# Kernel optimization log

Measured on AMD Instinct MI355X. Metric: run time of the kernel, lower is better.

Reference implementation:

```python
import jax, jax.numpy as jnp
import numpy as np

N, E, D, L = 50000, 600000, 128, 3
EPS = 1e-5


def _layer_norm(x, g, b):
    m = jnp.mean(x, axis=-1, keepdims=True)
    v = jnp.mean((x - m) ** 2, axis=-1, keepdims=True)
    return (x - m) * jax.lax.rsqrt(v + EPS) * g + b


def setup_inputs() -> dict:
    key = jax.random.key(0)
    ks = jax.random.split(key, 20)
    s = 1.0 / np.sqrt(D)
    inp = {
        "node": jax.random.normal(ks[0], (N, D), jnp.float32),
        "edge_attr": jax.random.uniform(ks[1], (E,), jnp.float32),
        # stacked per-layer parameters [L, ...]
        "W_rel": jax.random.uniform(ks[2], (L, D, D), jnp.float32, -s, s),
        "b_rel": jax.random.uniform(ks[3], (L, D), jnp.float32, -s, s),
        "W_root": jax.random.uniform(ks[4], (L, D, D), jnp.float32, -s, s),
        "ln1_g": jnp.ones((L, D), jnp.float32),
        "ln1_b": jnp.zeros((L, D), jnp.float32),
        "ln2_g": jnp.ones((L, D), jnp.float32),
        "ln2_b": jnp.zeros((L, D), jnp.float32),
        "W1": jax.random.uniform(ks[5], (L, D, D), jnp.float32, -s, s),
        "b1": jax.random.uniform(ks[6], (L, D), jnp.float32, -s, s),
        "W2": jax.random.uniform(ks[7], (L, D, D), jnp.float32, -s, s),
        "b2": jax.random.uniform(ks[8], (L, D), jnp.float32, -s, s),
        "jk_W": jax.random.uniform(ks[9], (L * D, D), jnp.float32, -1.0 / np.sqrt(L * D), 1.0 / np.sqrt(L * D)),
        "jk_b": jax.random.uniform(ks[10], (D,), jnp.float32, -1.0 / np.sqrt(L * D), 1.0 / np.sqrt(L * D)),
        "edge_index": jax.random.randint(ks[11], (2, E), 0, N, jnp.int64),
        "batch_ptr": jnp.sort(jax.random.randint(ks[12], (51,), 0, N, jnp.int64)),
    }
    return inp


def reference(node, edge_attr, W_rel, b_rel, W_root, ln1_g, ln1_b, ln2_g, ln2_b,
              W1, b1, W2, b2, jk_W, jk_b, edge_index, batch_ptr):
    src, dst = edge_index[0], edge_index[1]
    deg = jax.ops.segment_sum(jnp.ones((E,), node.dtype), dst, num_segments=N)
    inv_deg = 1.0 / jnp.maximum(deg, 1.0)  # nodes with no in-edges -> 0 aggregate
    outs = []
    for l in range(L):
        msg = node[src] * edge_attr[:, None]                       # [E, D] gather
        agg = jax.ops.segment_sum(msg, dst, num_segments=N)        # scatter-sum
        mean = agg * inv_deg[:, None]                              # mean aggregation
        # GraphConv: lin_rel(aggr) + lin_root(x); skip_connection=False
        node = mean @ W_rel[l] + b_rel[l] + node @ W_root[l]
        node = jax.nn.relu(_layer_norm(node @ W1[l] + b1[l], ln1_g[l], ln1_b[l]))
        node = jax.nn.relu(_layer_norm(node @ W2[l] + b2[l], ln2_g[l], ln2_b[l]))
        outs.append(node)
    jk = jnp.concatenate(outs, axis=-1)                            # [N, L*D]
    return jk @ jk_W + jk_b
```

## Files before the change

kernel.cpp:

```cpp
#include <hip/hip_runtime.h>

#define NN 50000
#define EE 600000
#define DD 128
#define CAP 64
#define SLDS_STRIDE 66
#define BINS 196
#define NP (BINS * 256)
#define BINCAP 3584
#define BCSTRIDE 16
#define LDS_STRIDE 136
#define P1_EDGES 2048
#define P1_BLOCKS ((EE + P1_EDGES - 1) / P1_EDGES)
#define CONV_BLKS 6250
#define PREP_BLKS (97 + CONV_BLKS)

typedef __attribute__((ext_vector_type(8))) short bf16x8;
typedef __attribute__((ext_vector_type(4))) float f32x4;

__device__ __forceinline__ unsigned short f2bf(float f) {
    union { float f; unsigned u; } v; v.f = f;
    unsigned r = v.u + 0x7FFF + ((v.u >> 16) & 1);
    return (unsigned short)(r >> 16);
}
__device__ __forceinline__ float bflo(unsigned x) { return __uint_as_float(x << 16); }
__device__ __forceinline__ float bfhi(unsigned x) { return __uint_as_float(x & 0xffff0000u); }

__global__ __launch_bounds__(256) void prep_fill(
    const float* __restrict__ nodef, unsigned short* __restrict__ node_bf,
    const float* __restrict__ W_rel, const float* __restrict__ W_root,
    const float* __restrict__ W1, const float* __restrict__ W2,
    const float* __restrict__ jkW,
    const float* __restrict__ b_rel, const float* __restrict__ b1,
    float* __restrict__ bc, unsigned short* __restrict__ packed,
    const int* __restrict__ src, const int* __restrict__ dst, const float* __restrict__ ea,
    int* __restrict__ binCnt, unsigned long long* __restrict__ recs) {
    __shared__ int hist[BINS];
    __shared__ int lstart[BINS];
    __shared__ int gbase[BINS];
    __shared__ int scan[256];
    __shared__ unsigned long long srt[P1_EDGES];
    const int b = blockIdx.x;
    const int t = threadIdx.x;

    if (b < 96) {
        int tg = b * 256 + t;
        int chunk = tg >> 11, r = tg & 2047;
        int lane = r & 63, tile = r >> 6;
        int kt = tile >> 3, nt = tile & 7;
        int quad = lane >> 4, n = lane & 15;
        int k0 = kt * 32 + quad * 8;
        int col = nt * 16 + n;
        union { unsigned short u[8]; uint4 v; } tmp;
        if (chunk < 6) {
            int l = (chunk < 3) ? chunk : chunk - 3;
            const float* A = ((chunk < 3) ? W_rel : W_root) + (size_t)l * 16384;
            const float* B = W1 + (size_t)l * 16384;
            float acc[8] = {0.f, 0.f, 0.f, 0.f, 0.f, 0.f, 0.f, 0.f};
            for (int k = 0; k < 128; ++k) {
                float bv = B[k * 128 + col];
#pragma unroll
                for (int j = 0; j < 8; ++j) acc[j] = fmaf(A[(k0 + j) * 128 + k], bv, acc[j]);
            }
#pragma unroll
            for (int j = 0; j < 8; ++j) tmp.u[j] = f2bf(acc[j]);
        } else {
            const float* s = (chunk < 9) ? (W2 + (size_t)(chunk - 6) * 16384)
                                         : (jkW + (size_t)(chunk - 9) * 16384);
#pragma unroll
            for (int j = 0; j < 8; ++j) tmp.u[j] = f2bf(s[(size_t)(k0 + j) * DD + col]);
        }
        *(uint4*)&packed[(size_t)tg * 8] = tmp.v;
        return;
    } else if (b == 96) {
        for (int o = t; o < 384; o += 256) {
            int l = o >> 7, j = o & 127;
            float s = 0.f;
            for (int k = 0; k < 128; ++k)
                s = fmaf(b_rel[l * 128 + k], W1[(size_t)l * 16384 + k * 128 + j], s);
            bc[o] = s + b1[o];
        }
        return;
    } else if (b < PREP_BLKS) {
        int i = (b - 97) * 256 + t;
        float4 v = *(const float4*)&nodef[(size_t)i * 4];
        ushort4 o;
        o.x = f2bf(v.x); o.y = f2bf(v.y); o.z = f2bf(v.z); o.w = f2bf(v.w);
        *(ushort4*)&node_bf[(size_t)i * 4] = o;
        return;
    }

    const int pb = b - PREP_BLKS;
    for (int i = t; i < BINS; i += 256) hist[i] = 0;
    __syncthreads();

    unsigned long long rec[8];
    int bin[8], rnk[8];
    bool val[8];
#pragma unroll
    for (int g = 0; g < 2; ++g) {
        int e0 = pb * P1_EDGES + g * 1024 + t * 4;
        int4 dv, sv; float4 ev;
        if (e0 + 3 < EE) {
            dv = *(const int4*)&dst[e0];
            sv = *(const int4*)&src[e0];
            ev = *(const float4*)&ea[e0];
        } else {
            int* dp = (int*)&dv; int* sp = (int*)&sv; float* ep = (float*)&ev;
#pragma unroll
            for (int k = 0; k < 4; ++k) {
                int e = e0 + k;
                dp[k] = (e < EE) ? dst[e] : 0;
                sp[k] = (e < EE) ? src[e] : 0;
                ep[k] = (e < EE) ? ea[e] : 0.f;
            }
        }
#pragma unroll
        for (int k = 0; k < 4; ++k) {
            int i = g * 4 + k;
            int e = e0 + k;
            val[i] = (e < EE);
            int d = ((const int*)&dv)[k];
            unsigned w16 = (unsigned)__float2int_rn(((const float*)&ev)[k] * 65535.0f);
            if (w16 > 65535u) w16 = 65535u;
            rec[i] = ((unsigned long long)(unsigned)d << 32) |
                     (((unsigned)((const int*)&sv)[k]) << 16) | w16;
            bin[i] = d >> 8;
            rnk[i] = val[i] ? atomicAdd(&hist[bin[i]], 1) : 0;
        }
    }
    __syncthreads();
    scan[t] = (t < BINS) ? hist[t] : 0;
    __syncthreads();
#pragma unroll
    for (int off = 1; off < 256; off <<= 1) {
        int v = (t >= off) ? scan[t - off] : 0;
        __syncthreads();
        scan[t] += v;
        __syncthreads();
    }
    if (t < BINS) {
        lstart[t] = scan[t] - hist[t];
        gbase[t] = hist[t] ? atomicAdd(&binCnt[t * BCSTRIDE], hist[t]) : 0;
    }
    __syncthreads();
#pragma unroll
    for (int i = 0; i < 8; ++i)
        if (val[i]) srt[lstart[bin[i]] + rnk[i]] = rec[i];
    __syncthreads();
    const int total = scan[255];
    for (int j = t; j < total; j += 256) {
        unsigned long long r = srt[j];
        int bb = (int)(r >> 40);
        int o = gbase[bb] + (j - lstart[bb]);
        if (o < BINCAP) recs[(size_t)bb * BINCAP + o] = r;
    }
}

__global__ __launch_bounds__(256) void fill_p2(
    const int* __restrict__ binCnt, const unsigned long long* __restrict__ recs,
    int* __restrict__ cnt, unsigned* __restrict__ slots) {
    __shared__ int cl[128];
    __shared__ unsigned sl[128 * CAP];
    const int b = blockIdx.x >> 1, half = blockIdx.x & 1, t = threadIdx.x;
    if (t < 128) cl[t] = 0;
    __syncthreads();
    int n = binCnt[b * BCSTRIDE];
    if (n > BINCAP) n = BINCAP;
    const unsigned long long* rp = recs + (size_t)b * BINCAP;
    for (int j = t; j < n; j += 256) {
        unsigned long long r = rp[j];
        int dl = (int)(r >> 32) & 255;
        if ((dl >> 7) == half) {
            int p = atomicAdd(&cl[dl & 127], 1);
            if (p < CAP) sl[(dl & 127) * CAP + p] = (unsigned)r;
        }
    }
    __syncthreads();
    const int node0 = (b << 8) + (half << 7);
    if (t < 128) cnt[node0 + t] = cl[t];
    const uint4* s4 = (const uint4*)sl;
    uint4* g4 = (uint4*)(slots + (size_t)node0 * CAP);
    for (int i = t; i < 2048; i += 256) g4[i] = s4[i];
}

template <bool JK>
__global__ __launch_bounds__(64, 4) void fused_layer(
    const unsigned short* __restrict__ feat,
    const unsigned* __restrict__ slots, const int* __restrict__ cnt,
    const unsigned short* __restrict__ PWrel, const unsigned short* __restrict__ PWroot,
    const unsigned short* __restrict__ PW2,
    const float* __restrict__ bc, const float* __restrict__ ln1g, const float* __restrict__ ln1b,
    const float* __restrict__ b2, const float* __restrict__ ln2g, const float* __restrict__ ln2b,
    unsigned short* __restrict__ out,
    const unsigned short* __restrict__ o0, const unsigned short* __restrict__ o1,
    const unsigned short* __restrict__ PJ0, const unsigned short* __restrict__ PJ1,
    const unsigned short* __restrict__ PJ2,
    const float* __restrict__ jkb, float* __restrict__ fout) {
    __shared__ __align__(16) unsigned short wt[16 * LDS_STRIDE];
    __shared__ __align__(16) unsigned slds[16 * SLDS_STRIDE];
    const int lane = threadIdx.x;
    const int mrow = blockIdx.x * 16;
    const int quad = lane >> 4, n15 = lane & 15;
    const int kq   = quad * 8;
    const int i8   = n15 * 8;
    const float wscale = 1.0f / 65535.0f;

    const int cl0 = cnt[mrow + n15];
    const int cAll = (cl0 > CAP) ? CAP : cl0;

    {
        const unsigned* sbase = slots + (size_t)mrow * CAP;
#pragma unroll
        for (int k = 0; k < 4; ++k) {
            int li = k * 64 + lane;
            uint4 v = *(const uint4*)&sbase[li * 4];
            int rw = li >> 4, cu = (li & 15) * 4;
            *(uint4*)&slds[rw * SLDS_STRIDE + cu] = v;
        }
    }

    const unsigned short* An = feat + (size_t)(mrow + n15) * DD;
    bf16x8 an4[4];
#pragma unroll
    for (int kt = 0; kt < 4; ++kt) an4[kt] = *(const bf16x8*)&An[kt * 32 + kq];

    __asm__ __volatile__("s_waitcnt lgkmcnt(0)" ::: "memory");

#pragma unroll
    for (int r = 0; r < 4; ++r) {
        const int row = r * 4 + quad;
        int c = __shfl(cAll, row);
        float acc[8] = {0.f, 0.f, 0.f, 0.f, 0.f, 0.f, 0.f, 0.f};
        for (int j0 = 0; j0 < c; j0 += 4) {
            uint4 sv = *(const uint4*)&slds[row * SLDS_STRIDE + j0];
            unsigned se[4] = {sv.x, sv.y, sv.z, sv.w};
#pragma unroll
            for (int tt = 0; tt < 4; ++tt) {
                bool ok = (j0 + tt) < c;
                unsigned e = se[tt];
                int   srcn = ok ? (int)(e >> 16) : 0;
                float w    = ok ? (float)(e & 0xffffu) * wscale : 0.0f;
                uint4 v = *(const uint4*)&feat[(size_t)srcn * DD + i8];
                acc[0] = fmaf(bflo(v.x), w, acc[0]);
                acc[1] = fmaf(bfhi(v.x), w, acc[1]);
                acc[2] = fmaf(bflo(v.y), w, acc[2]);
                acc[3] = fmaf(bfhi(v.y), w, acc[3]);
                acc[4] = fmaf(bflo(v.z), w, acc[4]);
                acc[5] = fmaf(bfhi(v.z), w, acc[5]);
                acc[6] = fmaf(bflo(v.w), w, acc[6]);
                acc[7] = fmaf(bfhi(v.w), w, acc[7]);
            }
        }
        float id = 1.0f / fmaxf((float)c, 1.0f);
        union { unsigned short u[8]; uint4 v; } o;
#pragma unroll
        for (int k = 0; k < 8; ++k) o.u[k] = f2bf(acc[k] * id);
        *(uint4*)&wt[row * LDS_STRIDE + i8] = o.v;
    }
    __asm__ __volatile__("s_waitcnt lgkmcnt(0)" ::: "memory");

    f32x4 acc[8];
#pragma unroll
    for (int nt = 0; nt < 8; ++nt) acc[nt] = (f32x4){0.f, 0.f, 0.f, 0.f};
    __builtin_amdgcn_s_setprio(1);
#pragma unroll
    for (int kt = 0; kt < 4; ++kt) {
        bf16x8 am = *(const bf16x8*)&wt[n15 * LDS_STRIDE + kt * 32 + kq];
#pragma unroll
        for (int nt = 0; nt < 8; ++nt) {
            bf16x8 brel = *(const bf16x8*)&PWrel[(size_t)((kt * 8 + nt) * 64 + lane) * 8];
            acc[nt] = __builtin_amdgcn_mfma_f32_16x16x32_bf16(am, brel, acc[nt], 0, 0, 0);
            bf16x8 brt = *(const bf16x8*)&PWroot[(size_t)((kt * 8 + nt) * 64 + lane) * 8];
            acc[nt] = __builtin_amdgcn_mfma_f32_16x16x32_bf16(an4[kt], brt, acc[nt], 0, 0, 0);
        }
    }
    __builtin_amdgcn_s_setprio(0);

    float x[8][4];
#pragma unroll
    for (int nt = 0; nt < 8; ++nt) {
        float bv = bc[nt * 16 + n15];
#pragma unroll
        for (int r = 0; r < 4; ++r) x[nt][r] = acc[nt][r] + bv;
    }
    {
        float s[4] = {0, 0, 0, 0}, q[4] = {0, 0, 0, 0};
#pragma unroll
        for (int nt = 0; nt < 8; ++nt)
#pragma unroll
            for (int r = 0; r < 4; ++r) { s[r] += x[nt][r]; q[r] += x[nt][r] * x[nt][r]; }
#pragma unroll
        for (int m = 1; m <= 8; m <<= 1)
#pragma unroll
            for (int r = 0; r < 4; ++r) { s[r] += __shfl_xor(s[r], m); q[r] += __shfl_xor(q[r], m); }
        const float inv = 1.0f / 128.0f;
#pragma unroll
        for (int r = 0; r < 4; ++r) {
            float mu = s[r] * inv;
            float rs = rsqrtf(fmaxf(q[r] * inv - mu * mu, 0.0f) + 1e-5f);
#pragma unroll
            for (int nt = 0; nt < 8; ++nt) {
                float g = ln1g[nt * 16 + n15], bb = ln1b[nt * 16 + n15];
                x[nt][r] = fmaxf((x[nt][r] - mu) * rs * g + bb, 0.0f);
            }
        }
    }

#pragma unroll
    for (int nt = 0; nt < 8; ++nt)
#pragma unroll
        for (int r = 0; r < 4; ++r)
            wt[(quad * 4 + r) * LDS_STRIDE + nt * 16 + n15] = f2bf(x[nt][r]);
    __asm__ __volatile__("s_waitcnt lgkmcnt(0)" ::: "memory");

    f32x4 acc2[8];
#pragma unroll
    for (int nt = 0; nt < 8; ++nt) acc2[nt] = (f32x4){0.f, 0.f, 0.f, 0.f};
    __builtin_amdgcn_s_setprio(1);
#pragma unroll
    for (int kt = 0; kt < 4; ++kt) {
        bf16x8 ah = *(const bf16x8*)&wt[n15 * LDS_STRIDE + kt * 32 + kq];
#pragma unroll
        for (int nt = 0; nt < 8; ++nt) {
            bf16x8 bw = *(const bf16x8*)&PW2[(size_t)((kt * 8 + nt) * 64 + lane) * 8];
            acc2[nt] = __builtin_amdgcn_mfma_f32_16x16x32_bf16(ah, bw, acc2[nt], 0, 0, 0);
        }
    }
    __builtin_amdgcn_s_setprio(0);
#pragma unroll
    for (int nt = 0; nt < 8; ++nt) {
        float bv = b2[nt * 16 + n15];
#pragma unroll
        for (int r = 0; r < 4; ++r) x[nt][r] = acc2[nt][r] + bv;
    }
    {
        float s[4] = {0, 0, 0, 0}, q[4] = {0, 0, 0, 0};
#pragma unroll
        for (int nt = 0; nt < 8; ++nt)
#pragma unroll
            for (int r = 0; r < 4; ++r) { s[r] += x[nt][r]; q[r] += x[nt][r] * x[nt][r]; }
#pragma unroll
        for (int m = 1; m <= 8; m <<= 1)
#pragma unroll
            for (int r = 0; r < 4; ++r) { s[r] += __shfl_xor(s[r], m); q[r] += __shfl_xor(q[r], m); }
        const float inv = 1.0f / 128.0f;
#pragma unroll
        for (int r = 0; r < 4; ++r) {
            float mu = s[r] * inv;
            float rs = rsqrtf(fmaxf(q[r] * inv - mu * mu, 0.0f) + 1e-5f);
#pragma unroll
            for (int nt = 0; nt < 8; ++nt) {
                float g = ln2g[nt * 16 + n15], bb = ln2b[nt * 16 + n15];
                x[nt][r] = fmaxf((x[nt][r] - mu) * rs * g + bb, 0.0f);
            }
        }
    }

    __asm__ __volatile__("s_waitcnt lgkmcnt(0)" ::: "memory");
#pragma unroll
    for (int nt = 0; nt < 8; ++nt)
#pragma unroll
        for (int r = 0; r < 4; ++r)
            wt[(quad * 4 + r) * LDS_STRIDE + nt * 16 + n15] = f2bf(x[nt][r]);
    __asm__ __volatile__("s_waitcnt lgkmcnt(0)" ::: "memory");

    if constexpr (!JK) {
#pragma unroll
        for (int i = 0; i < 4; ++i) {
            int s = i * 512 + lane * 8;
            int r = s >> 7, col = s & 127;
            uint4 v = *(const uint4*)&wt[r * LDS_STRIDE + col];
            *(uint4*)&out[(size_t)(mrow + r) * DD + col] = v;
        }
    } else {
        f32x4 accJ[8];
#pragma unroll
        for (int nt = 0; nt < 8; ++nt) accJ[nt] = (f32x4){0.f, 0.f, 0.f, 0.f};
        __builtin_amdgcn_s_setprio(1);
#pragma unroll
        for (int kt = 0; kt < 4; ++kt) {
            bf16x8 ah = *(const bf16x8*)&wt[n15 * LDS_STRIDE + kt * 32 + kq];
#pragma unroll
            for (int nt = 0; nt < 8; ++nt) {
                bf16x8 bw = *(const bf16x8*)&PJ2[(size_t)((kt * 8 + nt) * 64 + lane) * 8];
                accJ[nt] = __builtin_amdgcn_mfma_f32_16x16x32_bf16(ah, bw, accJ[nt], 0, 0, 0);
            }
        }
        const unsigned short* A0 = o0 + (size_t)(mrow + n15) * DD;
        const unsigned short* A1 = o1 + (size_t)(mrow + n15) * DD;
#pragma unroll
        for (int kt = 0; kt < 4; ++kt) {
            bf16x8 a0 = *(const bf16x8*)&A0[kt * 32 + kq];
            bf16x8 a1 = *(const bf16x8*)&A1[kt * 32 + kq];
#pragma unroll
            for (int nt = 0; nt < 8; ++nt) {
                bf16x8 b0 = *(const bf16x8*)&PJ0[(size_t)((kt * 8 + nt) * 64 + lane) * 8];
                accJ[nt] = __builtin_amdgcn_mfma_f32_16x16x32_bf16(a0, b0, accJ[nt], 0, 0, 0);
                bf16x8 b1 = *(const bf16x8*)&PJ1[(size_t)((kt * 8 + nt) * 64 + lane) * 8];
                accJ[nt] = __builtin_amdgcn_mfma_f32_16x16x32_bf16(a1, b1, accJ[nt], 0, 0, 0);
            }
        }
        __builtin_amdgcn_s_setprio(0);
#pragma unroll
        for (int nt = 0; nt < 8; ++nt) {
            float bv = jkb[nt * 16 + n15];
#pragma unroll
            for (int r = 0; r < 4; ++r)
                fout[(size_t)(mrow + quad * 4 + r) * DD + nt * 16 + n15] = accJ[nt][r] + bv;
        }
    }
}

extern "C" void kernel_launch(void* const* d_in, const int* in_sizes, int n_in,
                              void* d_out, int out_size, void* d_ws, size_t ws_size,
                              hipStream_t stream) {
    const float* node   = (const float*)d_in[0];
    const float* ea     = (const float*)d_in[1];
    const float* W_rel  = (const float*)d_in[2];
    const float* b_rel  = (const float*)d_in[3];
    const float* W_root = (const float*)d_in[4];
    const float* ln1_g  = (const float*)d_in[5];
    const float* ln1_b  = (const float*)d_in[6];
    const float* ln2_g  = (const float*)d_in[7];
    const float* ln2_b  = (const float*)d_in[8];
    const float* W1     = (const float*)d_in[9];
    const float* b1     = (const float*)d_in[10];
    const float* W2     = (const float*)d_in[11];
    const float* b2     = (const float*)d_in[12];
    const float* jk_W   = (const float*)d_in[13];
    const float* jk_b   = (const float*)d_in[14];
    const int*   ei     = (const int*)d_in[15];
    const int* srcI = ei;
    const int* dstI = ei + EE;

    char* ws = (char*)d_ws;
    size_t off = 0;
    auto alloc = [&](size_t bytes) {
        void* p = ws + off;
        off += (bytes + 255) & ~(size_t)255;
        return p;
    };
    int*                binCnt  = (int*)alloc((size_t)BINS * BCSTRIDE * 4);
    unsigned long long* recs    = (unsigned long long*)alloc((size_t)BINS * BINCAP * 8);
    int*                cnt     = (int*)alloc((size_t)NP * 4);
    unsigned*           slots   = (unsigned*)alloc((size_t)NP * CAP * 4);
    unsigned short*     node_bf = (unsigned short*)alloc((size_t)NN * DD * 2);
    unsigned short* outs_bf[2];
    for (int l = 0; l < 2; ++l) outs_bf[l] = (unsigned short*)alloc((size_t)NN * DD * 2);
    float*              bc      = (float*)alloc((size_t)3 * 128 * 4);
    unsigned short*     packed  = (unsigned short*)alloc((size_t)12 * 16384 * 2);

    hipMemsetAsync(binCnt, 0, (size_t)BINS * BCSTRIDE * 4, stream);
    prep_fill<<<PREP_BLKS + P1_BLOCKS, 256, 0, stream>>>(
        node, node_bf, W_rel, W_root, W1, W2, jk_W, b_rel, b1, bc, packed,
        srcI, dstI, ea, binCnt, recs);
    fill_p2<<<BINS * 2, 256, 0, stream>>>(binCnt, recs, cnt, slots);

    const int gblocks = NN / 16;
    unsigned short* cur = node_bf;
    for (int l = 0; l < 3; ++l) {
        if (l < 2) {
            fused_layer<false><<<gblocks, 64, 0, stream>>>(
                cur, slots, cnt,
                packed + (size_t)l * 16384, packed + (size_t)(3 + l) * 16384,
                packed + (size_t)(6 + l) * 16384,
                bc + (size_t)l * DD, ln1_g + (size_t)l * DD, ln1_b + (size_t)l * DD,
                b2 + (size_t)l * DD, ln2_g + (size_t)l * DD, ln2_b + (size_t)l * DD,
                outs_bf[l],
                nullptr, nullptr, nullptr, nullptr, nullptr, nullptr, nullptr);
            cur = outs_bf[l];
        } else {
            fused_layer<true><<<gblocks, 64, 0, stream>>>(
                cur, slots, cnt,
                packed + (size_t)l * 16384, packed + (size_t)(3 + l) * 16384,
                packed + (size_t)(6 + l) * 16384,
                bc + (size_t)l * DD, ln1_g + (size_t)l * DD, ln1_b + (size_t)l * DD,
                b2 + (size_t)l * DD, ln2_g + (size_t)l * DD, ln2_b + (size_t)l * DD,
                nullptr,
                outs_bf[0], outs_bf[1],
                packed + (size_t)9 * 16384, packed + (size_t)10 * 16384, packed + (size_t)11 * 16384,
                jk_b, (float*)d_out);
        }
    }
}
```

Before: 248.7 us.

## Fuse three layer launches into one persistent kernel with grid barriers

The three per-layer kernel launches are replaced by a single kernel that loops over the layers in-kernel. A software grid barrier separates the layers: 64 spread atomic counters, spin-polled with s_sleep and bracketed by thread fences. The aim is to remove the launch gaps and tail effects between layers, and to load each block's neighbor-slot table into LDS once instead of once per layer. In exchange it depends on all 3125 blocks being co-resident, and it risks deadlock or spin overhead if occupancy is lower than assumed.

New measurement: 967.0 us. 3.89x slower.

```diff
diff --git a/kernel.cpp b/kernel.cpp
--- a/kernel.cpp
+++ b/kernel.cpp
@@ -14,6 +14,7 @@
 #define P1_BLOCKS ((EE + P1_EDGES - 1) / P1_EDGES)
 #define CONV_BLKS 6250
 #define PREP_BLKS (97 + CONV_BLKS)
+#define GBLOCKS (NN / 16)
 
 typedef __attribute__((ext_vector_type(8))) short bf16x8;
 typedef __attribute__((ext_vector_type(4))) float f32x4;
@@ -25,6 +26,15 @@
 }
 __device__ __forceinline__ float bflo(unsigned x) { return __uint_as_float(x << 16); }
 __device__ __forceinline__ float bfhi(unsigned x) { return __uint_as_float(x & 0xffff0000u); }
+
+__device__ __forceinline__ void gbar(int* bar, int lane, int bid) {
+    __threadfence();
+    if (lane == 0) atomicAdd(&bar[bid & 63], 1);
+    const int expct = (lane < 53) ? 49 : 48;
+    while (__hip_atomic_load(&bar[lane], __ATOMIC_RELAXED, __HIP_MEMORY_SCOPE_AGENT) < expct)
+        __builtin_amdgcn_s_sleep(16);
+    __threadfence();
+}
 
 __global__ __launch_bounds__(256) void prep_fill(
     const float* __restrict__ nodef, unsigned short* __restrict__ node_bf,
@@ -184,23 +194,19 @@
     for (int i = t; i < 2048; i += 256) g4[i] = s4[i];
 }
 
-template <bool JK>
-__global__ __launch_bounds__(64, 4) void fused_layer(
-    const unsigned short* __restrict__ feat,
+__global__ __launch_bounds__(64, 4) void fused_all(
+    const unsigned short* __restrict__ node_bf,
     const unsigned* __restrict__ slots, const int* __restrict__ cnt,
-    const unsigned short* __restrict__ PWrel, const unsigned short* __restrict__ PWroot,
-    const unsigned short* __restrict__ PW2,
-    const float* __restrict__ bc, const float* __restrict__ ln1g, const float* __restrict__ ln1b,
-    const float* __restrict__ b2, const float* __restrict__ ln2g, const float* __restrict__ ln2b,
-    unsigned short* __restrict__ out,
-    const unsigned short* __restrict__ o0, const unsigned short* __restrict__ o1,
-    const unsigned short* __restrict__ PJ0, const unsigned short* __restrict__ PJ1,
-    const unsigned short* __restrict__ PJ2,
-    const float* __restrict__ jkb, float* __restrict__ fout) {
+    const unsigned short* __restrict__ packed,
+    const float* __restrict__ bcA, const float* __restrict__ ln1gA, const float* __restrict__ ln1bA,
+    const float* __restrict__ b2A, const float* __restrict__ ln2gA, const float* __restrict__ ln2bA,
+    unsigned short* __restrict__ out0, unsigned short* __restrict__ out1,
+    const float* __restrict__ jkb, float* __restrict__ fout, int* __restrict__ bars) {
     __shared__ __align__(16) unsigned short wt[16 * LDS_STRIDE];
     __shared__ __align__(16) unsigned slds[16 * SLDS_STRIDE];
     const int lane = threadIdx.x;
-    const int mrow = blockIdx.x * 16;
+    const int bid  = blockIdx.x;
+    const int mrow = bid * 16;
     const int quad = lane >> 4, n15 = lane & 15;
     const int kq   = quad * 8;
     const int i8   = n15 * 8;
@@ -220,194 +226,212 @@
         }
     }
 
-    const unsigned short* An = feat + (size_t)(mrow + n15) * DD;
-    bf16x8 an4[4];
-#pragma unroll
-    for (int kt = 0; kt < 4; ++kt) an4[kt] = *(const bf16x8*)&An[kt * 32 + kq];
-
-    __asm__ __volatile__("s_waitcnt lgkmcnt(0)" ::: "memory");
-
-#pragma unroll
-    for (int r = 0; r < 4; ++r) {
-        const int row = r * 4 + quad;
-        int c = __shfl(cAll, row);
-        float acc[8] = {0.f, 0.f, 0.f, 0.f, 0.f, 0.f, 0.f, 0.f};
-        for (int j0 = 0; j0 < c; j0 += 4) {
-            uint4 sv = *(const uint4*)&slds[row * SLDS_STRIDE + j0];
-            unsigned se[4] = {sv.x, sv.y, sv.z, sv.w};
-#pragma unroll
-            for (int tt = 0; tt < 4; ++tt) {
-                bool ok = (j0 + tt) < c;
-                unsigned e = se[tt];
-                int   srcn = ok ? (int)(e >> 16) : 0;
-                float w    = ok ? (float)(e & 0xffffu) * wscale : 0.0f;
-                uint4 v = *(const uint4*)&feat[(size_t)srcn * DD + i8];
-                acc[0] = fmaf(bflo(v.x), w, acc[0]);
-                acc[1] = fmaf(bfhi(v.x), w, acc[1]);
-                acc[2] = fmaf(bflo(v.y), w, acc[2]);
-                acc[3] = fmaf(bfhi(v.y), w, acc[3]);
-                acc[4] = fmaf(bflo(v.z), w, acc[4]);
-                acc[5] = fmaf(bfhi(v.z), w, acc[5]);
-                acc[6] = fmaf(bflo(v.w), w, acc[6]);
-                acc[7] = fmaf(bfhi(v.w), w, acc[7]);
-            }
-        }
-        float id = 1.0f / fmaxf((float)c, 1.0f);
-        union { unsigned short u[8]; uint4 v; } o;
-#pragma unroll
-        for (int k = 0; k < 8; ++k) o.u[k] = f2bf(acc[k] * id);
-        *(uint4*)&wt[row * LDS_STRIDE + i8] = o.v;
-    }
-    __asm__ __volatile__("s_waitcnt lgkmcnt(0)" ::: "memory");
-
-    f32x4 acc[8];
-#pragma unroll
-    for (int nt = 0; nt < 8; ++nt) acc[nt] = (f32x4){0.f, 0.f, 0.f, 0.f};
-    __builtin_amdgcn_s_setprio(1);
-#pragma unroll
-    for (int kt = 0; kt < 4; ++kt) {
-        bf16x8 am = *(const bf16x8*)&wt[n15 * LDS_STRIDE + kt * 32 + kq];
+    for (int l = 0; l < 3; ++l) {
+        const unsigned short* feat  = (l == 0) ? node_bf : ((l == 1) ? out0 : out1);
+        const unsigned short* PWrel  = packed + (size_t)l * 16384;
+        const unsigned short* PWroot = packed + (size_t)(3 + l) * 16384;
+        const unsigned short* PW2    = packed + (size_t)(6 + l) * 16384;
+        const float* bc   = bcA   + l * 128;
+        const float* ln1g = ln1gA + l * 128;
+        const float* ln1b = ln1bA + l * 128;
+        const float* b2   = b2A   + l * 128;
+        const float* ln2g = ln2gA + l * 128;
+        const float* ln2b = ln2bA + l * 128;
+
+        const unsigned short* An = feat + (size_t)(mrow + n15) * DD;
+        bf16x8 an4[4];
+#pragma unroll
+        for (int kt = 0; kt < 4; ++kt) an4[kt] = *(const bf16x8*)&An[kt * 32 + kq];
+
+        __asm__ __volatile__("s_waitcnt lgkmcnt(0)" ::: "memory");
+
+#pragma unroll
+        for (int r = 0; r < 4; ++r) {
+            const int row = r * 4 + quad;
+            int c = __shfl(cAll, row);
+            float acc[8] = {0.f, 0.f, 0.f, 0.f, 0.f, 0.f, 0.f, 0.f};
+            for (int j0 = 0; j0 < c; j0 += 4) {
+                uint4 sv = *(const uint4*)&slds[row * SLDS_STRIDE + j0];
+                unsigned se[4] = {sv.x, sv.y, sv.z, sv.w};
+#pragma unroll
+                for (int tt = 0; tt < 4; ++tt) {
+                    bool ok = (j0 + tt) < c;
+                    unsigned e = se[tt];
+                    int   srcn = ok ? (int)(e >> 16) : 0;
+                    float w    = ok ? (float)(e & 0xffffu) * wscale : 0.0f;
+                    uint4 v = *(const uint4*)&feat[(size_t)srcn * DD + i8];
+                    acc[0] = fmaf(bflo(v.x), w, acc[0]);
+                    acc[1] = fmaf(bfhi(v.x), w, acc[1]);
+                    acc[2] = fmaf(bflo(v.y), w, acc[2]);
+                    acc[3] = fmaf(bfhi(v.y), w, acc[3]);
+                    acc[4] = fmaf(bflo(v.z), w, acc[4]);
+                    acc[5] = fmaf(bfhi(v.z), w, acc[5]);
+                    acc[6] = fmaf(bflo(v.w), w, acc[6]);
+                    acc[7] = fmaf(bfhi(v.w), w, acc[7]);
+                }
+            }
+            float id = 1.0f / fmaxf((float)c, 1.0f);
+            union { unsigned short u[8]; uint4 v; } o;
+#pragma unroll
+            for (int k = 0; k < 8; ++k) o.u[k] = f2bf(acc[k] * id);
+            *(uint4*)&wt[row * LDS_STRIDE + i8] = o.v;
+        }
+        __asm__ __volatile__("s_waitcnt lgkmcnt(0)" ::: "memory");
+
+        f32x4 acc[8];
+#pragma unroll
+        for (int nt = 0; nt < 8; ++nt) acc[nt] = (f32x4){0.f, 0.f, 0.f, 0.f};
+        __builtin_amdgcn_s_setprio(1);
+#pragma unroll
+        for (int kt = 0; kt < 4; ++kt) {
+            bf16x8 am = *(const bf16x8*)&wt[n15 * LDS_STRIDE + kt * 32 + kq];
+#pragma unroll
+            for (int nt = 0; nt < 8; ++nt) {
+                bf16x8 brel = *(const bf16x8*)&PWrel[(size_t)((kt * 8 + nt) * 64 + lane) * 8];
+                acc[nt] = __builtin_amdgcn_mfma_f32_16x16x32_bf16(am, brel, acc[nt], 0, 0, 0);
+                bf16x8 brt = *(const bf16x8*)&PWroot[(size_t)((kt * 8 + nt) * 64 + lane) * 8];
+                acc[nt] = __builtin_amdgcn_mfma_f32_16x16x32_bf16(an4[kt], brt, acc[nt], 0, 0, 0);
+            }
+        }
+        __builtin_amdgcn_s_setprio(0);
+
+        float x[8][4];
 #pragma unroll
         for (int nt = 0; nt < 8; ++nt) {
-            bf16x8 brel = *(const bf16x8*)&PWrel[(size_t)((kt * 8 + nt) * 64 + lane) * 8];
-            acc[nt] = __builtin_amdgcn_mfma_f32_16x16x32_bf16(am, brel, acc[nt], 0, 0, 0);
-            bf16x8 brt = *(const bf16x8*)&PWroot[(size_t)((kt * 8 + nt) * 64 + lane) * 8];
-            acc[nt] = __builtin_amdgcn_mfma_f32_16x16x32_bf16(an4[kt], brt, acc[nt], 0, 0, 0);
-        }
-    }
-    __builtin_amdgcn_s_setprio(0);
-
-    float x[8][4];
-#pragma unroll
-    for (int nt = 0; nt < 8; ++nt) {
-        float bv = bc[nt * 16 + n15];
-#pragma unroll
-        for (int r = 0; r < 4; ++r) x[nt][r] = acc[nt][r] + bv;
-    }
-    {
-        float s[4] = {0, 0, 0, 0}, q[4] = {0, 0, 0, 0};
+            float bv = bc[nt * 16 + n15];
+#pragma unroll
+            for (int r = 0; r < 4; ++r) x[nt][r] = acc[nt][r] + bv;
+        }
+        {
+            float s[4] = {0, 0, 0, 0}, q[4] = {0, 0, 0, 0};
+#pragma unroll
+            for (int nt = 0; nt < 8; ++nt)
+#pragma unroll
+                for (int r = 0; r < 4; ++r) { s[r] += x[nt][r]; q[r] += x[nt][r] * x[nt][r]; }
+#pragma unroll
+            for (int m = 1; m <= 8; m <<= 1)
+#pragma unroll
+                for (int r = 0; r < 4; ++r) { s[r] += __shfl_xor(s[r], m); q[r] += __shfl_xor(q[r], m); }
+            const float inv = 1.0f / 128.0f;
+#pragma unroll
+            for (int r = 0; r < 4; ++r) {
+                float mu = s[r] * inv;
+                float rs = rsqrtf(fmaxf(q[r] * inv - mu * mu, 0.0f) + 1e-5f);
+#pragma unroll
+                for (int nt = 0; nt < 8; ++nt) {
+                    float g = ln1g[nt * 16 + n15], bb = ln1b[nt * 16 + n15];
+                    x[nt][r] = fmaxf((x[nt][r] - mu) * rs * g + bb, 0.0f);
+                }
+            }
+        }
+
 #pragma unroll
         for (int nt = 0; nt < 8; ++nt)
 #pragma unroll
-            for (int r = 0; r < 4; ++r) { s[r] += x[nt][r]; q[r] += x[nt][r] * x[nt][r]; }
-#pragma unroll
-        for (int m = 1; m <= 8; m <<= 1)
-#pragma unroll
-            for (int r = 0; r < 4; ++r) { s[r] += __shfl_xor(s[r], m); q[r] += __shfl_xor(q[r], m); }
-        const float inv = 1.0f / 128.0f;
-#pragma unroll
-        for (int r = 0; r < 4; ++r) {
-            float mu = s[r] * inv;
-            float rs = rsqrtf(fmaxf(q[r] * inv - mu * mu, 0.0f) + 1e-5f);
-#pragma unroll
-            for (int nt = 0; nt < 8; ++nt) {
-                float g = ln1g[nt * 16 + n15], bb = ln1b[nt * 16 + n15];
-                x[nt][r] = fmaxf((x[nt][r] - mu) * rs * g + bb, 0.0f);
-            }
-        }
-    }
-
-#pragma unroll
-    for (int nt = 0; nt < 8; ++nt)
-#pragma unroll
-        for (int r = 0; r < 4; ++r)
-            wt[(quad * 4 + r) * LDS_STRIDE + nt * 16 + n15] = f2bf(x[nt][r]);
-    __asm__ __volatile__("s_waitcnt lgkmcnt(0)" ::: "memory");
-
-    f32x4 acc2[8];
-#pragma unroll
-    for (int nt = 0; nt < 8; ++nt) acc2[nt] = (f32x4){0.f, 0.f, 0.f, 0.f};
-    __builtin_amdgcn_s_setprio(1);
-#pragma unroll
-    for (int kt = 0; kt < 4; ++kt) {
-        bf16x8 ah = *(const bf16x8*)&wt[n15 * LDS_STRIDE + kt * 32 + kq];
-#pragma unroll
-        for (int nt = 0; nt < 8; ++nt) {
-            bf16x8 bw = *(const bf16x8*)&PW2[(size_t)((kt * 8 + nt) * 64 + lane) * 8];
-            acc2[nt] = __builtin_amdgcn_mfma_f32_16x16x32_bf16(ah, bw, acc2[nt], 0, 0, 0);
-        }
-    }
-    __builtin_amdgcn_s_setprio(0);
-#pragma unroll
-    for (int nt = 0; nt < 8; ++nt) {
-        float bv = b2[nt * 16 + n15];
-#pragma unroll
-        for (int r = 0; r < 4; ++r) x[nt][r] = acc2[nt][r] + bv;
-    }
-    {
-        float s[4] = {0, 0, 0, 0}, q[4] = {0, 0, 0, 0};
-#pragma unroll
-        for (int nt = 0; nt < 8; ++nt)
-#pragma unroll
-            for (int r = 0; r < 4; ++r) { s[r] += x[nt][r]; q[r] += x[nt][r] * x[nt][r]; }
-#pragma unroll
-        for (int m = 1; m <= 8; m <<= 1)
-#pragma unroll
-            for (int r = 0; r < 4; ++r) { s[r] += __shfl_xor(s[r], m); q[r] += __shfl_xor(q[r], m); }
-        const float inv = 1.0f / 128.0f;
-#pragma unroll
-        for (int r = 0; r < 4; ++r) {
-            float mu = s[r] * inv;
-            float rs = rsqrtf(fmaxf(q[r] * inv - mu * mu, 0.0f) + 1e-5f);
-#pragma unroll
-            for (int nt = 0; nt < 8; ++nt) {
-                float g = ln2g[nt * 16 + n15], bb = ln2b[nt * 16 + n15];
-                x[nt][r] = fmaxf((x[nt][r] - mu) * rs * g + bb, 0.0f);
-            }
-        }
-    }
-
-    __asm__ __volatile__("s_waitcnt lgkmcnt(0)" ::: "memory");
-#pragma unroll
-    for (int nt = 0; nt < 8; ++nt)
-#pragma unroll
-        for (int r = 0; r < 4; ++r)
-            wt[(quad * 4 + r) * LDS_STRIDE + nt * 16 + n15] = f2bf(x[nt][r]);
-    __asm__ __volatile__("s_waitcnt lgkmcnt(0)" ::: "memory");
-
-    if constexpr (!JK) {
-#pragma unroll
-        for (int i = 0; i < 4; ++i) {
-            int s = i * 512 + lane * 8;
-            int r = s >> 7, col = s & 127;
-            uint4 v = *(const uint4*)&wt[r * LDS_STRIDE + col];
-            *(uint4*)&out[(size_t)(mrow + r) * DD + col] = v;
-        }
-    } else {
-        f32x4 accJ[8];
-#pragma unroll
-        for (int nt = 0; nt < 8; ++nt) accJ[nt] = (f32x4){0.f, 0.f, 0.f, 0.f};
+            for (int r = 0; r < 4; ++r)
+                wt[(quad * 4 + r) * LDS_STRIDE + nt * 16 + n15] = f2bf(x[nt][r]);
+        __asm__ __volatile__("s_waitcnt lgkmcnt(0)" ::: "memory");
+
+        f32x4 acc2[8];
+#pragma unroll
+        for (int nt = 0; nt < 8; ++nt) acc2[nt] = (f32x4){0.f, 0.f, 0.f, 0.f};
         __builtin_amdgcn_s_setprio(1);
 #pragma unroll
         for (int kt = 0; kt < 4; ++kt) {
             bf16x8 ah = *(const bf16x8*)&wt[n15 * LDS_STRIDE + kt * 32 + kq];
 #pragma unroll
             for (int nt = 0; nt < 8; ++nt) {
-                bf16x8 bw = *(const bf16x8*)&PJ2[(size_t)((kt * 8 + nt) * 64 + lane) * 8];
-                accJ[nt] = __builtin_amdgcn_mfma_f32_16x16x32_bf16(ah, bw, accJ[nt], 0, 0, 0);
-            }
-        }
-        const unsigned short* A0 = o0 + (size_t)(mrow + n15) * DD;
-        const unsigned short* A1 = o1 + (size_t)(mrow + n15) * DD;
-#pragma unroll
-        for (int kt = 0; kt < 4; ++kt) {
-            bf16x8 a0 = *(const bf16x8*)&A0[kt * 32 + kq];
-            bf16x8 a1 = *(const bf16x8*)&A1[kt * 32 + kq];
+                bf16x8 bw = *(const bf16x8*)&PW2[(size_t)((kt * 8 + nt) * 64 + lane) * 8];
+                acc2[nt] = __builtin_amdgcn_mfma_f32_16x16x32_bf16(ah, bw, acc2[nt], 0, 0, 0);
+            }
+        }
+        __builtin_amdgcn_s_setprio(0);
+#pragma unroll
+        for (int nt = 0; nt < 8; ++nt) {
+            float bv = b2[nt * 16 + n15];
+#pragma unroll
+            for (int r = 0; r < 4; ++r) x[nt][r] = acc2[nt][r] + bv;
+        }
+        {
+            float s[4] = {0, 0, 0, 0}, q[4] = {0, 0, 0, 0};
+#pragma unroll
+            for (int nt = 0; nt < 8; ++nt)
+#pragma unroll
+                for (int r = 0; r < 4; ++r) { s[r] += x[nt][r]; q[r] += x[nt][r] * x[nt][r]; }
+#pragma unroll
+            for (int m = 1; m <= 8; m <<= 1)
+#pragma unroll
+                for (int r = 0; r < 4; ++r) { s[r] += __shfl_xor(s[r], m); q[r] += __shfl_xor(q[r], m); }
+            const float inv = 1.0f / 128.0f;
+#pragma unroll
+            for (int r = 0; r < 4; ++r) {
+                float mu = s[r] * inv;
+                float rs = rsqrtf(fmaxf(q[r] * inv - mu * mu, 0.0f) + 1e-5f);
+#pragma unroll
+                for (int nt = 0; nt < 8; ++nt) {
+                    float g = ln2g[nt * 16 + n15], bb = ln2b[nt * 16 + n15];
+                    x[nt][r] = fmaxf((x[nt][r] - mu) * rs * g + bb, 0.0f);
+                }
+            }
+        }
+
+        __asm__ __volatile__("s_waitcnt lgkmcnt(0)" ::: "memory");
+#pragma unroll
+        for (int nt = 0; nt < 8; ++nt)
+#pragma unroll
+            for (int r = 0; r < 4; ++r)
+                wt[(quad * 4 + r) * LDS_STRIDE + nt * 16 + n15] = f2bf(x[nt][r]);
+        __asm__ __volatile__("s_waitcnt lgkmcnt(0)" ::: "memory");
+
+        if (l < 2) {
+            unsigned short* out = (l == 0) ? out0 : out1;
+#pragma unroll
+            for (int i = 0; i < 4; ++i) {
+                int s = i * 512 + lane * 8;
+                int r = s >> 7, col = s & 127;
+                uint4 v = *(const uint4*)&wt[r * LDS_STRIDE + col];
+                *(uint4*)&out[(size_t)(mrow + r) * DD + col] = v;
+            }
+            gbar(bars + l * 64, lane, bid);
+        } else {
+            const unsigned short* PJ0 = packed + (size_t)9  * 16384;
+            const unsigned short* PJ1 = packed + (size_t)10 * 16384;
+            const unsigned short* PJ2 = packed + (size_t)11 * 16384;
+            f32x4 accJ[8];
+#pragma unroll
+            for (int nt = 0; nt < 8; ++nt) accJ[nt] = (f32x4){0.f, 0.f, 0.f, 0.f};
+            __builtin_amdgcn_s_setprio(1);
+#pragma unroll
+            for (int kt = 0; kt < 4; ++kt) {
+                bf16x8 ah = *(const bf16x8*)&wt[n15 * LDS_STRIDE + kt * 32 + kq];
+#pragma unroll
+                for (int nt = 0; nt < 8; ++nt) {
+                    bf16x8 bw = *(const bf16x8*)&PJ2[(size_t)((kt * 8 + nt) * 64 + lane) * 8];
+                    accJ[nt] = __builtin_amdgcn_mfma_f32_16x16x32_bf16(ah, bw, accJ[nt], 0, 0, 0);
+                }
+            }
+            const unsigned short* A0 = out0 + (size_t)(mrow + n15) * DD;
+            const unsigned short* A1 = out1 + (size_t)(mrow + n15) * DD;
+#pragma unroll
+            for (int kt = 0; kt < 4; ++kt) {
+                bf16x8 a0 = *(const bf16x8*)&A0[kt * 32 + kq];
+                bf16x8 a1 = *(const bf16x8*)&A1[kt * 32 + kq];
+#pragma unroll
+                for (int nt = 0; nt < 8; ++nt) {
+                    bf16x8 b0 = *(const bf16x8*)&PJ0[(size_t)((kt * 8 + nt) * 64 + lane) * 8];
+                    accJ[nt] = __builtin_amdgcn_mfma_f32_16x16x32_bf16(a0, b0, accJ[nt], 0, 0, 0);
+                    bf16x8 b1 = *(const bf16x8*)&PJ1[(size_t)((kt * 8 + nt) * 64 + lane) * 8];
+                    accJ[nt] = __builtin_amdgcn_mfma_f32_16x16x32_bf16(a1, b1, accJ[nt], 0, 0, 0);
+                }
+            }
+            __builtin_amdgcn_s_setprio(0);
 #pragma unroll
             for (int nt = 0; nt < 8; ++nt) {
-                bf16x8 b0 = *(const bf16x8*)&PJ0[(size_t)((kt * 8 + nt) * 64 + lane) * 8];
-                accJ[nt] = __builtin_amdgcn_mfma_f32_16x16x32_bf16(a0, b0, accJ[nt], 0, 0, 0);
-                bf16x8 b1 = *(const bf16x8*)&PJ1[(size_t)((kt * 8 + nt) * 64 + lane) * 8];
-                accJ[nt] = __builtin_amdgcn_mfma_f32_16x16x32_bf16(a1, b1, accJ[nt], 0, 0, 0);
-            }
-        }
-        __builtin_amdgcn_s_setprio(0);
-#pragma unroll
-        for (int nt = 0; nt < 8; ++nt) {
-            float bv = jkb[nt * 16 + n15];
-#pragma unroll
-            for (int r = 0; r < 4; ++r)
-                fout[(size_t)(mrow + quad * 4 + r) * DD + nt * 16 + n15] = accJ[nt][r] + bv;
+                float bv = jkb[nt * 16 + n15];
+#pragma unroll
+                for (int r = 0; r < 4; ++r)
+                    fout[(size_t)(mrow + quad * 4 + r) * DD + nt * 16 + n15] = accJ[nt][r] + bv;
+            }
         }
     }
 }
@@ -441,46 +465,24 @@
         off += (bytes + 255) & ~(size_t)255;
         return p;
     };
+    int*                bars    = (int*)alloc((size_t)2 * 64 * 4);
     int*                binCnt  = (int*)alloc((size_t)BINS * BCSTRIDE * 4);
     unsigned long long* recs    = (unsigned long long*)alloc((size_t)BINS * BINCAP * 8);
     int*                cnt     = (int*)alloc((size_t)NP * 4);
     unsigned*           slots   = (unsigned*)alloc((size_t)NP * CAP * 4);
     unsigned short*     node_bf = (unsigned short*)alloc((size_t)NN * DD * 2);
-    unsigned short* outs_bf[2];
-    for (int l = 0; l < 2; ++l) outs_bf[l] = (unsigned short*)alloc((size_t)NN * DD * 2);
+    unsigned short*     out0    = (unsigned short*)alloc((size_t)NN * DD * 2);
+    unsigned short*     out1    = (unsigned short*)alloc((size_t)NN * DD * 2);
     float*              bc      = (float*)alloc((size_t)3 * 128 * 4);
     unsigned short*     packed  = (unsigned short*)alloc((size_t)12 * 16384 * 2);
 
-    hipMemsetAsync(binCnt, 0, (size_t)BINS * BCSTRIDE * 4, stream);
+    hipMemsetAsync(bars, 0, (size_t)2 * 64 * 4 + (size_t)BINS * BCSTRIDE * 4, stream);
     prep_fill<<<PREP_BLKS + P1_BLOCKS, 256, 0, stream>>>(
         node, node_bf, W_rel, W_root, W1, W2, jk_W, b_rel, b1, bc, packed,
         srcI, dstI, ea, binCnt, recs);
     fill_p2<<<BINS * 2, 256, 0, stream>>>(binCnt, recs, cnt, slots);
-
-    const int gblocks = NN / 16;
-    unsigned short* cur = node_bf;
-    for (int l = 0; l < 3; ++l) {
-        if (l < 2) {
-            fused_layer<false><<<gblocks, 64, 0, stream>>>(
-                cur, slots, cnt,
-                packed + (size_t)l * 16384, packed + (size_t)(3 + l) * 16384,
-                packed + (size_t)(6 + l) * 16384,
-                bc + (size_t)l * DD, ln1_g + (size_t)l * DD, ln1_b + (size_t)l * DD,
-                b2 + (size_t)l * DD, ln2_g + (size_t)l * DD, ln2_b + (size_t)l * DD,
-                outs_bf[l],
-                nullptr, nullptr, nullptr, nullptr, nullptr, nullptr, nullptr);
-            cur = outs_bf[l];
-        } else {
-            fused_layer<true><<<gblocks, 64, 0, stream>>>(
-                cur, slots, cnt,
-                packed + (size_t)l * 16384, packed + (size_t)(3 + l) * 16384,
-                packed + (size_t)(6 + l) * 16384,
-                bc + (size_t)l * DD, ln1_g + (size_t)l * DD, ln1_b + (size_t)l * DD,
-                b2 + (size_t)l * DD, ln2_g + (size_t)l * DD, ln2_b + (size_t)l * DD,
-                nullptr,
-                outs_bf[0], outs_bf[1],
-                packed + (size_t)9 * 16384, packed + (size_t)10 * 16384, packed + (size_t)11 * 16384,
-                jk_b, (float*)d_out);
-        }
-    }
-}
+    fused_all<<<GBLOCKS, 64, 0, stream>>>(
+        node_bf, slots, cnt, packed,
+        bc, ln1_g, ln1_b, b2, ln2_g, ln2_b,
+        out0, out1, jk_b, (float*)d_out, bars);
+}
```

## Process 32 rows per wavefront so each weight fragment feeds two MFMAs

Applied to the files above, without the earlier changes.

Each single-wave block in fused_layer now handles 32 node rows as two 16-row halves instead of 16 rows. Every packed weight fragment loaded from global memory is used for two MFMAs, which halves weight-load traffic per row and halves the number of blocks. The cost is more accumulator registers, with occupancy lowered from 4 to 3 waves in the launch bounds, plus bounds guards for the padded tail rows since 50000 is not a multiple of 32.

Measured after the change: 270.9 us. 8.9% more time.

```diff
diff --git a/kernel.cpp b/kernel.cpp
--- a/kernel.cpp
+++ b/kernel.cpp
@@ -4,6 +4,7 @@
 #define EE 600000
 #define DD 128
 #define CAP 64
+#define TROWS 32
 #define SLDS_STRIDE 66
 #define BINS 196
 #define NP (BINS * 256)
@@ -185,7 +186,7 @@
 }
 
 template <bool JK>
-__global__ __launch_bounds__(64, 4) void fused_layer(
+__global__ __launch_bounds__(64, 3) void fused_layer(
     const unsigned short* __restrict__ feat,
     const unsigned* __restrict__ slots, const int* __restrict__ cnt,
     const unsigned short* __restrict__ PWrel, const unsigned short* __restrict__ PWroot,
@@ -197,22 +198,22 @@
     const unsigned short* __restrict__ PJ0, const unsigned short* __restrict__ PJ1,
     const unsigned short* __restrict__ PJ2,
     const float* __restrict__ jkb, float* __restrict__ fout) {
-    __shared__ __align__(16) unsigned short wt[16 * LDS_STRIDE];
-    __shared__ __align__(16) unsigned slds[16 * SLDS_STRIDE];
+    __shared__ __align__(16) unsigned short wt[TROWS * LDS_STRIDE];
+    __shared__ __align__(16) unsigned slds[TROWS * SLDS_STRIDE];
     const int lane = threadIdx.x;
-    const int mrow = blockIdx.x * 16;
+    const int mrow = blockIdx.x * TROWS;
     const int quad = lane >> 4, n15 = lane & 15;
     const int kq   = quad * 8;
     const int i8   = n15 * 8;
     const float wscale = 1.0f / 65535.0f;
 
-    const int cl0 = cnt[mrow + n15];
+    const int cl0 = cnt[mrow + lane];
     const int cAll = (cl0 > CAP) ? CAP : cl0;
 
     {
         const unsigned* sbase = slots + (size_t)mrow * CAP;
 #pragma unroll
-        for (int k = 0; k < 4; ++k) {
+        for (int k = 0; k < 8; ++k) {
             int li = k * 64 + lane;
             uint4 v = *(const uint4*)&sbase[li * 4];
             int rw = li >> 4, cu = (li & 15) * 4;
@@ -220,15 +221,20 @@
         }
     }
 
-    const unsigned short* An = feat + (size_t)(mrow + n15) * DD;
-    bf16x8 an4[4];
-#pragma unroll
-    for (int kt = 0; kt < 4; ++kt) an4[kt] = *(const bf16x8*)&An[kt * 32 + kq];
+    bf16x8 an4[2][4];
+#pragma unroll
+    for (int h = 0; h < 2; ++h) {
+        int arow = mrow + h * 16 + n15;
+        if (arow >= NN) arow = NN - 1;
+        const unsigned short* An = feat + (size_t)arow * DD;
+#pragma unroll
+        for (int kt = 0; kt < 4; ++kt) an4[h][kt] = *(const bf16x8*)&An[kt * 32 + kq];
+    }
 
     __asm__ __volatile__("s_waitcnt lgkmcnt(0)" ::: "memory");
 
 #pragma unroll
-    for (int r = 0; r < 4; ++r) {
+    for (int r = 0; r < 8; ++r) {
         const int row = r * 4 + quad;
         int c = __shfl(cAll, row);
         float acc[8] = {0.f, 0.f, 0.f, 0.f, 0.f, 0.f, 0.f, 0.f};
@@ -260,31 +266,37 @@
     }
     __asm__ __volatile__("s_waitcnt lgkmcnt(0)" ::: "memory");
 
-    f32x4 acc[8];
-#pragma unroll
-    for (int nt = 0; nt < 8; ++nt) acc[nt] = (f32x4){0.f, 0.f, 0.f, 0.f};
+    f32x4 acc1[2][8];
+#pragma unroll
+    for (int h = 0; h < 2; ++h)
+#pragma unroll
+        for (int nt = 0; nt < 8; ++nt) acc1[h][nt] = (f32x4){0.f, 0.f, 0.f, 0.f};
     __builtin_amdgcn_s_setprio(1);
 #pragma unroll
     for (int kt = 0; kt < 4; ++kt) {
-        bf16x8 am = *(const bf16x8*)&wt[n15 * LDS_STRIDE + kt * 32 + kq];
+        bf16x8 am0 = *(const bf16x8*)&wt[n15 * LDS_STRIDE + kt * 32 + kq];
+        bf16x8 am1 = *(const bf16x8*)&wt[(16 + n15) * LDS_STRIDE + kt * 32 + kq];
 #pragma unroll
         for (int nt = 0; nt < 8; ++nt) {
             bf16x8 brel = *(const bf16x8*)&PWrel[(size_t)((kt * 8 + nt) * 64 + lane) * 8];
-            acc[nt] = __builtin_amdgcn_mfma_f32_16x16x32_bf16(am, brel, acc[nt], 0, 0, 0);
+            acc1[0][nt] = __builtin_amdgcn_mfma_f32_16x16x32_bf16(am0, brel, acc1[0][nt], 0, 0, 0);
+            acc1[1][nt] = __builtin_amdgcn_mfma_f32_16x16x32_bf16(am1, brel, acc1[1][nt], 0, 0, 0);
             bf16x8 brt = *(const bf16x8*)&PWroot[(size_t)((kt * 8 + nt) * 64 + lane) * 8];
-            acc[nt] = __builtin_amdgcn_mfma_f32_16x16x32_bf16(an4[kt], brt, acc[nt], 0, 0, 0);
+            acc1[0][nt] = __builtin_amdgcn_mfma_f32_16x16x32_bf16(an4[0][kt], brt, acc1[0][nt], 0, 0, 0);
+            acc1[1][nt] = __builtin_amdgcn_mfma_f32_16x16x32_bf16(an4[1][kt], brt, acc1[1][nt], 0, 0, 0);
         }
     }
     __builtin_amdgcn_s_setprio(0);
 
-    float x[8][4];
-#pragma unroll
-    for (int nt = 0; nt < 8; ++nt) {
-        float bv = bc[nt * 16 + n15];
-#pragma unroll
-        for (int r = 0; r < 4; ++r) x[nt][r] = acc[nt][r] + bv;
-    }
-    {
+#pragma unroll
+    for (int h = 0; h < 2; ++h) {
+        float x[8][4];
+#pragma unroll
+        for (int nt = 0; nt < 8; ++nt) {
+            float bv = bc[nt * 16 + n15];
+#pragma unroll
+            for (int r = 0; r < 4; ++r) x[nt][r] = acc1[h][nt][r] + bv;
+        }
         float s[4] = {0, 0, 0, 0}, q[4] = {0, 0, 0, 0};
 #pragma unroll
         for (int nt = 0; nt < 8; ++nt)
@@ -305,36 +317,43 @@
                 x[nt][r] = fmaxf((x[nt][r] - mu) * rs * g + bb, 0.0f);
             }
         }
-    }
-
-#pragma unroll
-    for (int nt = 0; nt < 8; ++nt)
-#pragma unroll
-        for (int r = 0; r < 4; ++r)
-            wt[(quad * 4 + r) * LDS_STRIDE + nt * 16 + n15] = f2bf(x[nt][r]);
+#pragma unroll
+        for (int nt = 0; nt < 8; ++nt)
+#pragma unroll
+            for (int r = 0; r < 4; ++r)
+                wt[(h * 16 + quad * 4 + r) * LDS_STRIDE + nt * 16 + n15] = f2bf(x[nt][r]);
+    }
     __asm__ __volatile__("s_waitcnt lgkmcnt(0)" ::: "memory");
 
-    f32x4 acc2[8];
-#pragma unroll
-    for (int nt = 0; nt < 8; ++nt) acc2[nt] = (f32x4){0.f, 0.f, 0.f, 0.f};
+    f32x4 acc2[2][8];
+#pragma unroll
+    for (int h = 0; h < 2; ++h)
+#pragma unroll
+        for (int nt = 0; nt < 8; ++nt) acc2[h][nt] = (f32x4){0.f, 0.f, 0.f, 0.f};
     __builtin_amdgcn_s_setprio(1);
 #pragma unroll
     for (int kt = 0; kt < 4; ++kt) {
-        bf16x8 ah = *(const bf16x8*)&wt[n15 * LDS_STRIDE + kt * 32 + kq];
+        bf16x8 ah0 = *(const bf16x8*)&wt[n15 * LDS_STRIDE + kt * 32 + kq];
+        bf16x8 ah1 = *(const bf16x8*)&wt[(16 + n15) * LDS_STRIDE + kt * 32 + kq];
 #pragma unroll
         for (int nt = 0; nt < 8; ++nt) {
             bf16x8 bw = *(const bf16x8*)&PW2[(size_t)((kt * 8 + nt) * 64 + lane) * 8];
-            acc2[nt] = __builtin_amdgcn_mfma_f32_16x16x32_bf16(ah, bw, acc2[nt], 0, 0, 0);
+            acc2[0][nt] = __builtin_amdgcn_mfma_f32_16x16x32_bf16(ah0, bw, acc2[0][nt], 0, 0, 0);
+            acc2[1][nt] = __builtin_amdgcn_mfma_f32_16x16x32_bf16(ah1, bw, acc2[1][nt], 0, 0, 0);
         }
     }
     __builtin_amdgcn_s_setprio(0);
-#pragma unroll
-    for (int nt = 0; nt < 8; ++nt) {
-        float bv = b2[nt * 16 + n15];
-#pragma unroll
-        for (int r = 0; r < 4; ++r) x[nt][r] = acc2[nt][r] + bv;
-    }
-    {
+
+    __asm__ __volatile__("s_waitcnt lgkmcnt(0)" ::: "memory");
+#pragma unroll
+    for (int h = 0; h < 2; ++h) {
+        float x[8][4];
+#pragma unroll
+        for (int nt = 0; nt < 8; ++nt) {
+            float bv = b2[nt * 16 + n15];
+#pragma unroll
+            for (int r = 0; r < 4; ++r) x[nt][r] = acc2[h][nt][r] + bv;
+        }
         float s[4] = {0, 0, 0, 0}, q[4] = {0, 0, 0, 0};
 #pragma unroll
         for (int nt = 0; nt < 8; ++nt)
@@ -355,60 +374,82 @@
                 x[nt][r] = fmaxf((x[nt][r] - mu) * rs * g + bb, 0.0f);
             }
         }
-    }
-
+#pragma unroll
+        for (int nt = 0; nt < 8; ++nt)
+#pragma unroll
+            for (int r = 0; r < 4; ++r)
+                wt[(h * 16 + quad * 4 + r) * LDS_STRIDE + nt * 16 + n15] = f2bf(x[nt][r]);
+    }
     __asm__ __volatile__("s_waitcnt lgkmcnt(0)" ::: "memory");
-#pragma unroll
-    for (int nt = 0; nt < 8; ++nt)
-#pragma unroll
-        for (int r = 0; r < 4; ++r)
-            wt[(quad * 4 + r) * LDS_STRIDE + nt * 16 + n15] = f2bf(x[nt][r]);
-    __asm__ __volatile__("s_waitcnt lgkmcnt(0)" ::: "memory");
 
     if constexpr (!JK) {
 #pragma unroll
-        for (int i = 0; i < 4; ++i) {
+        for (int i = 0; i < 8; ++i) {
             int s = i * 512 + lane * 8;
             int r = s >> 7, col = s & 127;
-            uint4 v = *(const uint4*)&wt[r * LDS_STRIDE + col];
-            *(uint4*)&out[(size_t)(mrow + r) * DD + col] = v;
+            if (mrow + r < NN) {
+                uint4 v = *(const uint4*)&wt[r * LDS_STRIDE + col];
+                *(uint4*)&out[(size_t)(mrow + r) * DD + col] = v;
+            }
         }
     } else {
-        f32x4 accJ[8];
-#pragma unroll
-        for (int nt = 0; nt < 8; ++nt) accJ[nt] = (f32x4){0.f, 0.f, 0.f, 0.f};
+        f32x4 accJ[2][8];
+#pragma unroll
+        for (int h = 0; h < 2; ++h)
+#pragma unroll
+            for (int nt = 0; nt < 8; ++nt) accJ[h][nt] = (f32x4){0.f, 0.f, 0.f, 0.f};
+        const unsigned short* A0p[2];
+        const unsigned short* A1p[2];
+#pragma unroll
+        for (int h = 0; h < 2; ++h) {
+            int arow = mrow + h * 16 + n15;
+            if (arow >= NN) arow = NN - 1;
+            A0p[h] = o0 + (size_t)arow * DD;
+            A1p[h] = o1 + (size_t)arow * DD;
+        }
         __builtin_amdgcn_s_setprio(1);
 #pragma unroll
         for (int kt = 0; kt < 4; ++kt) {
-            bf16x8 ah = *(const bf16x8*)&wt[n15 * LDS_STRIDE + kt * 32 + kq];
+            bf16x8 ah0 = *(const bf16x8*)&wt[n15 * LDS_STRIDE + kt * 32 + kq];
+            bf16x8 ah1 = *(const bf16x8*)&wt[(16 + n15) * LDS_STRIDE + kt * 32 + kq];
 #pragma unroll
             for (int nt = 0; nt < 8; ++nt) {
                 bf16x8 bw = *(const bf16x8*)&PJ2[(size_t)((kt * 8 + nt) * 64 + lane) * 8];
-                accJ[nt] = __builtin_amdgcn_mfma_f32_16x16x32_bf16(ah, bw, accJ[nt], 0, 0, 0);
-            }
-        }
-        const unsigned short* A0 = o0 + (size_t)(mrow + n15) * DD;
-        const unsigned short* A1 = o1 + (size_t)(mrow + n15) * DD;
+                accJ[0][nt] = __builtin_amdgcn_mfma_f32_16x16x32_bf16(ah0, bw, accJ[0][nt], 0, 0, 0);
+                accJ[1][nt] = __builtin_amdgcn_mfma_f32_16x16x32_bf16(ah1, bw, accJ[1][nt], 0, 0, 0);
+            }
+        }
 #pragma unroll
         for (int kt = 0; kt < 4; ++kt) {
-            bf16x8 a0 = *(const bf16x8*)&A0[kt * 32 + kq];
-            bf16x8 a1 = *(const bf16x8*)&A1[kt * 32 + kq];
+            bf16x8 a0h[2], a1h[2];
+#pragma unroll
+            for (int h = 0; h < 2; ++h) {
+                a0h[h] = *(const bf16x8*)&A0p[h][kt * 32 + kq];
+                a1h[h] = *(const bf16x8*)&A1p[h][kt * 32 + kq];
+            }
 #pragma unroll
             for (int nt = 0; nt < 8; ++nt) {
                 bf16x8 b0 = *(const bf16x8*)&PJ0[(size_t)((kt * 8 + nt) * 64 + lane) * 8];
-                accJ[nt] = __builtin_amdgcn_mfma_f32_16x16x32_bf16(a0, b0, accJ[nt], 0, 0, 0);
+                accJ[0][nt] = __builtin_amdgcn_mfma_f32_16x16x32_bf16(a0h[0], b0, accJ[0][nt], 0, 0, 0);
+                accJ[1][nt] = __builtin_amdgcn_mfma_f32_16x16x32_bf16(a0h[1], b0, accJ[1][nt], 0, 0, 0);
                 bf16x8 b1 = *(const bf16x8*)&PJ1[(size_t)((kt * 8 + nt) * 64 + lane) * 8];
-                accJ[nt] = __builtin_amdgcn_mfma_f32_16x16x32_bf16(a1, b1, accJ[nt], 0, 0, 0);
+                accJ[0][nt] = __builtin_amdgcn_mfma_f32_16x16x32_bf16(a1h[0], b1, accJ[0][nt], 0, 0, 0);
+                accJ[1][nt] = __builtin_amdgcn_mfma_f32_16x16x32_bf16(a1h[1], b1, accJ[1][nt], 0, 0, 0);
             }
         }
         __builtin_amdgcn_s_setprio(0);
 #pragma unroll
-        for (int nt = 0; nt < 8; ++nt) {
-            float bv = jkb[nt * 16 + n15];
-#pragma unroll
-            for (int r = 0; r < 4; ++r)
-                fout[(size_t)(mrow + quad * 4 + r) * DD + nt * 16 + n15] = accJ[nt][r] + bv;
-        }
+        for (int h = 0; h < 2; ++h)
+#pragma unroll
+            for (int nt = 0; nt < 8; ++nt) {
+                float bv = jkb[nt * 16 + n15];
+#pragma unroll
+                for (int r = 0; r < 4; ++r) {
+                    int row = mrow + h * 16 + quad * 4 + r;
+                    if (row < NN)
+                        fout[(size_t)row * DD + nt * 16 + n15] = accJ[h][nt][r] + bv;
+                }
+            }
     }
 }
 
@@ -457,7 +498,7 @@
         srcI, dstI, ea, binCnt, recs);
     fill_p2<<<BINS * 2, 256, 0, stream>>>(binCnt, recs, cnt, slots);
 
-    const int gblocks = NN / 16;
+    const int gblocks = (NN + TROWS - 1) / TROWS;
     unsigned short* cur = node_bf;
     for (int l = 0; l < 3; ++l) {
         if (l < 2) {
```
